# Optimization experiments

Hardware: AMD Instinct MI355X
Metric: run time of the kernel (lower is better)

The kernel has to match this reference:

```python
import jax, jax.numpy as jnp
import numpy as np

B, T, S, A, P = 256, 32, 2048, 64, 128


def setup_inputs() -> dict:
    key = jax.random.key(0)
    ks = jax.random.split(key, 10)
    def w(k, shape, fan_in):
        return jax.random.normal(k, shape, dtype=jnp.float32) / np.sqrt(fan_in)
    return {
        "state": jax.random.normal(ks[0], (B, S), dtype=jnp.float32),
        "act_sequence": jax.random.normal(ks[1], (B, T, A), dtype=jnp.float32),
        "latent": jax.random.normal(ks[2], (B, P), dtype=jnp.float32),
        "fc_W": w(ks[3], (S, S + A + P), S + A + P),
        "fc_b": jnp.zeros((S,), dtype=jnp.float32),
        "fc1_W": w(ks[4], (S, 2 * S), 2 * S),
        "fc2_W": w(ks[5], (S, S), S),
        "W_W": w(ks[6], (4 * S, S), S),
        "reward_W": w(ks[7], (1, S), S),
        "reward_b": jnp.zeros((1,), dtype=jnp.float32),
    }


def reference(state, act_sequence, latent, fc_W, fc_b, fc1_W, fc2_W, W_W, reward_W, reward_b):
    s_dim = fc2_W.shape[0]
    relu = jax.nn.relu

    def fc(x):  # nn.Linear(s+a+p -> s, bias=True)
        return x @ fc_W.T + fc_b

    # initial hidden/cell both from relu(fc(cat[state, act[:,0], latent]))
    hs0 = jnp.concatenate([state, act_sequence[:, 0, :], latent], axis=1)
    hidden = relu(fc(hs0))
    cell = relu(fc(hs0))

    acts = jnp.transpose(act_sequence, (1, 0, 2))  # [T, B, A]

    def step(carry, act_i):
        h, c = carry
        # LSTMCell called as lstm(hidden, [hidden, cell]) -> input == h_cur == h
        combined = jnp.concatenate([h, h], axis=1)            # [B, 2S]
        x = relu(combined @ fc1_W.T)
        x = relu(x @ fc2_W.T)
        cc = relu(x @ W_W.T)                                   # [B, 4S]
        cc_i, cc_f, cc_o, cc_g = jnp.split(cc, 4, axis=1)
        i_g = jax.nn.sigmoid(cc_i)
        f_g = jax.nn.sigmoid(cc_f)
        o_g = jax.nn.sigmoid(cc_o)
        g_g = jnp.tanh(cc_g)
        c_next = f_g * c + i_g * g_g
        h_next = o_g * jnp.tanh(c_next)
        reward = h_next @ reward_W.T + reward_b                # [B, 1]
        # hidden for next iteration (uses act_sequence[:, i, :], as in source);
        # at the last step this carry is simply discarded.
        hs = jnp.concatenate([h_next, act_i, latent], axis=1)
        h_carry = relu(fc(hs))
        return (h_carry, c_next), (h_next, reward)

    (_, _), (preds, rewards) = jax.lax.scan(step, (hidden, cell), acts)
    # torch.cat(list, dim=0) over T steps of [B, *] -> [T*B, *]
    preds = preds.reshape(-1, s_dim)
    rewards = rewards.reshape(-1, 1)
    return preds, rewards
```

## Files before the change

### kernel.cpp

```cpp
#include <hip/hip_runtime.h>

typedef unsigned short u16;
typedef unsigned int   u32;
typedef __attribute__((ext_vector_type(8))) short s8v;
typedef __attribute__((ext_vector_type(8))) unsigned short u8v;
typedef __attribute__((ext_vector_type(4))) float f32x4;

__device__ __forceinline__ float bf2f(u16 v) {
    union { u32 u; float f; } x; x.u = ((u32)v) << 16; return x.f;
}
__device__ __forceinline__ u16 f2bf(float f) {
    union { float f; u32 u; } x; x.f = f;
    return (u16)((x.u + 0x7fffu + ((x.u >> 16) & 1u)) >> 16);
}
__device__ __forceinline__ float sigf(float x)  { return 1.0f / (1.0f + __expf(-x)); }
__device__ __forceinline__ float tanhf_(float x){ return 1.0f - 2.0f / (__expf(2.0f * x) + 1.0f); }

constexpr int Bb = 256, Tt = 32, Ss = 2048, Aa = 64, Pp = 128, SAPd = 2240;

typedef const __attribute__((address_space(1))) unsigned int* gp1_t;
typedef __attribute__((address_space(3))) unsigned int* lp3_t;
__device__ __forceinline__ void gl16(const void* g, void* l) {
    __builtin_amdgcn_global_load_lds((gp1_t)g, (lp3_t)l, 16, 0, 0);
}
#define VMW3() asm volatile("s_waitcnt vmcnt(3)" ::: "memory")
#define VMW0() asm volatile("s_waitcnt vmcnt(0)" ::: "memory")

__global__ void detect_k(const u32* __restrict__ st, int* __restrict__ flag) {
    u32 w = st[threadIdx.x];
    int e = (w >> 7) & 0xFF;
    unsigned long long m = __ballot(e >= 100 && e <= 140);
    if (threadIdx.x == 0) flag[0] = (__popcll(m) >= 32) ? 1 : 0;
}

__global__ __launch_bounds__(256)
void prep_k(const void* __restrict__ state, const void* __restrict__ act,
            const void* __restrict__ latent, const void* __restrict__ fc1W,
            u16* __restrict__ hs, u16* __restrict__ fc1s, float* __restrict__ rewbuf,
            const int* __restrict__ flagp, int big)
{
    const bool bfe = (flagp[0] == 1);
    int g0 = blockIdx.x * 256 + threadIdx.x;
    int stride = gridDim.x * 256;
    for (int i = g0; i < Bb * SAPd; i += stride) {
        int b = i / SAPd, k = i - b * SAPd;
        const void* p; size_t src;
        if (k < Ss)           { p = state;  src = (size_t)b * Ss + k; }
        else if (k < Ss + Aa) { p = act;    src = (size_t)b * (Tt * Aa) + (k - Ss); }
        else                  { p = latent; src = (size_t)b * Pp + (k - Ss - Aa); }
        hs[i] = bfe ? ((const u16*)p)[src] : f2bf(((const float*)p)[src]);
    }
    for (int i = g0; i < Tt * Bb; i += stride) rewbuf[i] = 0.0f;
    if (big) {
        for (int i = g0; i < Ss * Ss; i += stride) {
            int n = i >> 11, k = i & 2047;
            float s;
            if (bfe) s = bf2f(((const u16*)fc1W)[(size_t)n * 4096 + k])
                       + bf2f(((const u16*)fc1W)[(size_t)n * 4096 + 2048 + k]);
            else     s = ((const float*)fc1W)[(size_t)n * 4096 + k]
                       + ((const float*)fc1W)[(size_t)n * 4096 + 2048 + k];
            fc1s[i] = f2bf(s);
        }
    }
}

template<int K, bool BIAS, bool WC, bool FOLD, bool ACT, bool WBF>
__global__ __launch_bounds__(256)
void gemm_k(const u16* __restrict__ Ap, const void* __restrict__ Wp,
            const void* __restrict__ biasp, u16* __restrict__ outp,
            float* __restrict__ cellp,
            u16* __restrict__ hsp, const void* __restrict__ actp, int t,
            const int* __restrict__ flagp)
{
    constexpr int NK = K / 64;
    __shared__ __align__(16) char smem[36864];
    const bool bfe = (flagp[0] == 1);
    const int tid = threadIdx.x;
    const int lane = tid & 63, w = tid >> 6, m16 = lane & 15, q = lane >> 4;
    const int r0 = blockIdx.y * 32, c0 = blockIdx.x * 64;

    if (ACT) {
        if (blockIdx.y == 0) {
            int i = blockIdx.x * 512 + tid * 2;
            int b = i >> 6, a2 = i & 63;
            if (bfe) {
                u32 v = *(const u32*)((const u16*)actp + ((size_t)b * Tt + t) * Aa + a2);
                *(u32*)(hsp + (size_t)b * SAPd + Ss + a2) = v;
            } else {
                const float* s = (const float*)actp + ((size_t)b * Tt + t) * Aa + a2;
                *(u32*)(hsp + (size_t)b * SAPd + Ss + a2) =
                    (u32)f2bf(s[0]) | ((u32)f2bf(s[1]) << 16);
            }
            VMW0();
        }
    }

    const int srow = tid >> 3, sch = tid & 7;
    const int fr2 = 32 + srow;
    f32x4 acc0 = {}, acc1 = {};
    const bool mainp = (WBF || bfe) && !FOLD;

    auto COMPUTE = [&](int p) {
        const char* bufA = smem + p * 12288;
        const char* bufB = bufA + 4096;
        const int sw = (m16 & 7) << 4;
        #pragma unroll
        for (int kh = 0; kh < 2; kh++) {
            int cb = ((kh << 6) | (q << 4)) ^ sw;
            s8v b  = *(const s8v*)(bufB + (w * 16 + m16) * 128 + cb);
            s8v a0 = *(const s8v*)(bufA + m16 * 128 + cb);
            s8v a1 = *(const s8v*)(bufA + (16 + m16) * 128 + cb);
            acc0 = __builtin_amdgcn_mfma_f32_16x16x32_bf16(a0, b, acc0, 0, 0, 0);
            acc1 = __builtin_amdgcn_mfma_f32_16x16x32_bf16(a1, b, acc1, 0, 0, 0);
        }
    };

    if (mainp) {
        const u16* W16 = (const u16*)Wp;
        auto STAGE = [&](int kt, int p) {
            char* bufA = smem + p * 12288;
            char* bufB = bufA + 4096;
            int kb = kt * 64;
            gl16(Ap + (size_t)(r0 + srow) * K + kb + ((sch ^ (srow & 7)) * 8),
                 bufA + w * 1024);
            gl16(W16 + (size_t)(c0 + srow) * K + kb + ((sch ^ (srow & 7)) * 8),
                 bufB + w * 1024);
            gl16(W16 + (size_t)(c0 + fr2) * K + kb + ((sch ^ (fr2 & 7)) * 8),
                 bufB + 4096 + w * 1024);
        };
        STAGE(0, 0); STAGE(1, 1);
        for (int k = 0; k < NK - 2; k++) {
            VMW3();
            __builtin_amdgcn_s_barrier();
            STAGE(k + 2, (k + 2) % 3);
            COMPUTE(k % 3);
        }
        VMW3();
        __builtin_amdgcn_s_barrier();
        COMPUTE((NK - 2) % 3);
        VMW0();
        __builtin_amdgcn_s_barrier();
        COMPUTE((NK - 1) % 3);
    } else {
        u8v fa; u8v rbh[4]; float4 rff[8];
        auto ISSUE = [&](int kt) {
            int kb = kt * 64;
            fa = *(const u8v*)(Ap + (size_t)(r0 + srow) * K + kb + sch * 8);
            if (FOLD) {
                if (bfe) {
                    const u16* p1 = (const u16*)Wp + (size_t)(c0 + srow) * (2 * K) + kb + sch * 8;
                    rbh[0] = *(const u8v*)p1; rbh[1] = *(const u8v*)(p1 + K);
                    const u16* p2 = (const u16*)Wp + (size_t)(c0 + fr2) * (2 * K) + kb + sch * 8;
                    rbh[2] = *(const u8v*)p2; rbh[3] = *(const u8v*)(p2 + K);
                } else {
                    const float* p1 = (const float*)Wp + (size_t)(c0 + srow) * (2 * K) + kb + sch * 8;
                    rff[0] = *(const float4*)p1;       rff[1] = *(const float4*)(p1 + 4);
                    rff[2] = *(const float4*)(p1 + K); rff[3] = *(const float4*)(p1 + K + 4);
                    const float* p2 = (const float*)Wp + (size_t)(c0 + fr2) * (2 * K) + kb + sch * 8;
                    rff[4] = *(const float4*)p2;       rff[5] = *(const float4*)(p2 + 4);
                    rff[6] = *(const float4*)(p2 + K); rff[7] = *(const float4*)(p2 + K + 4);
                }
            } else {
                const float* p1 = (const float*)Wp + (size_t)(c0 + srow) * K + kb + sch * 8;
                rff[0] = *(const float4*)p1; rff[1] = *(const float4*)(p1 + 4);
                const float* p2 = (const float*)Wp + (size_t)(c0 + fr2) * K + kb + sch * 8;
                rff[2] = *(const float4*)p2; rff[3] = *(const float4*)(p2 + 4);
            }
        };
        auto COMMIT = [&](int p) {
            char* bufA = smem + p * 12288;
            char* bufB = bufA + 4096;
            *(u8v*)(bufA + srow * 128 + ((sch ^ (srow & 7)) * 16)) = fa;
            u8v v1, v2;
            if (FOLD) {
                if (bfe) {
                    #pragma unroll
                    for (int j = 0; j < 8; j++) {
                        v1[j] = f2bf(bf2f(rbh[0][j]) + bf2f(rbh[1][j]));
                        v2[j] = f2bf(bf2f(rbh[2][j]) + bf2f(rbh[3][j]));
                    }
                } else {
                    float a0[8], a1[8], b0[8], b1[8];
                    *(float4*)&a0[0] = rff[0]; *(float4*)&a0[4] = rff[1];
                    *(float4*)&a1[0] = rff[2]; *(float4*)&a1[4] = rff[3];
                    *(float4*)&b0[0] = rff[4]; *(float4*)&b0[4] = rff[5];
                    *(float4*)&b1[0] = rff[6]; *(float4*)&b1[4] = rff[7];
                    #pragma unroll
                    for (int j = 0; j < 8; j++) {
                        v1[j] = f2bf(a0[j] + a1[j]);
                        v2[j] = f2bf(b0[j] + b1[j]);
                    }
                }
            } else {
                float a0[8], a1[8];
                *(float4*)&a0[0] = rff[0]; *(float4*)&a0[4] = rff[1];
                *(float4*)&a1[0] = rff[2]; *(float4*)&a1[4] = rff[3];
                #pragma unroll
                for (int j = 0; j < 8; j++) { v1[j] = f2bf(a0[j]); v2[j] = f2bf(a1[j]); }
            }
            *(u8v*)(bufB + srow * 128 + ((sch ^ (srow & 7)) * 16)) = v1;
            *(u8v*)(bufB + fr2 * 128 + ((sch ^ (fr2 & 7)) * 16)) = v2;
        };
        ISSUE(0);
        for (int k = 0; k < NK; k++) {
            __syncthreads();
            COMMIT(k & 1);
            __syncthreads();
            if (k + 1 < NK) ISSUE(k + 1);
            COMPUTE(k & 1);
        }
    }

    const int col = c0 + w * 16 + m16;
    float bv = 0.0f;
    if (BIAS) bv = bfe ? bf2f(((const u16*)biasp)[col]) : ((const float*)biasp)[col];
    #pragma unroll
    for (int r = 0; r < 4; r++) {
        int row0 = r0 + q * 4 + r;
        float v0 = fmaxf(acc0[r] + bv, 0.0f);
        outp[(size_t)row0 * 2048 + col] = f2bf(v0);
        if (WC) cellp[(size_t)row0 * 2048 + col] = v0;
        int row1 = r0 + 16 + q * 4 + r;
        float v1 = fmaxf(acc1[r] + bv, 0.0f);
        outp[(size_t)row1 * 2048 + col] = f2bf(v1);
        if (WC) cellp[(size_t)row1 * 2048 + col] = v1;
    }
}

__global__ __launch_bounds__(256)
void wgates_k(const u16* __restrict__ Ap, const void* __restrict__ Wp,
              float* __restrict__ cbuf, u16* __restrict__ hsp,
              void* __restrict__ dout, const void* __restrict__ rwWp,
              float* __restrict__ rewbuf, int t, const int* __restrict__ flagp)
{
    constexpr int K = 2048, NK = 32;
    __shared__ __align__(16) char smem[36864];
    const bool bfe = (flagp[0] == 1);
    const int tid = threadIdx.x;
    const int lane = tid & 63, g = tid >> 6, m16 = lane & 15, q = lane >> 4;
    const int r0 = blockIdx.y * 32, j0 = blockIdx.x * 16;

    const int srow = tid >> 3, sch = tid & 7;
    const int fr2 = 32 + srow;
    const int wr1 = (srow >> 4) * 2048 + j0 + (srow & 15);
    const int wr2 = (fr2 >> 4) * 2048 + j0 + (fr2 & 15);
    f32x4 acc0 = {}, acc1 = {};

    auto COMPUTE = [&](int p) {
        const char* bufA = smem + p * 12288;
        const char* bufB = bufA + 4096;
        const int sw = (m16 & 7) << 4;
        #pragma unroll
        for (int kh = 0; kh < 2; kh++) {
            int cb = ((kh << 6) | (q << 4)) ^ sw;
            s8v b  = *(const s8v*)(bufB + (g * 16 + m16) * 128 + cb);
            s8v a0 = *(const s8v*)(bufA + m16 * 128 + cb);
            s8v a1 = *(const s8v*)(bufA + (16 + m16) * 128 + cb);
            acc0 = __builtin_amdgcn_mfma_f32_16x16x32_bf16(a0, b, acc0, 0, 0, 0);
            acc1 = __builtin_amdgcn_mfma_f32_16x16x32_bf16(a1, b, acc1, 0, 0, 0);
        }
    };

    if (bfe) {
        const u16* W16 = (const u16*)Wp;
        auto STAGE = [&](int kt, int p) {
            char* bufA = smem + p * 12288;
            char* bufB = bufA + 4096;
            int kb = kt * 64;
            gl16(Ap + (size_t)(r0 + srow) * K + kb + ((sch ^ (srow & 7)) * 8),
                 bufA + g * 1024);
            gl16(W16 + (size_t)wr1 * K + kb + ((sch ^ (srow & 7)) * 8),
                 bufB + g * 1024);
            gl16(W16 + (size_t)wr2 * K + kb + ((sch ^ (fr2 & 7)) * 8),
                 bufB + 4096 + g * 1024);
        };
        STAGE(0, 0); STAGE(1, 1);
        for (int k = 0; k < NK - 2; k++) {
            VMW3();
            __builtin_amdgcn_s_barrier();
            STAGE(k + 2, (k + 2) % 3);
            COMPUTE(k % 3);
        }
        VMW3();
        __builtin_amdgcn_s_barrier();
        COMPUTE((NK - 2) % 3);
        VMW0();
        __builtin_amdgcn_s_barrier();
        COMPUTE((NK - 1) % 3);
    } else {
        u8v fa; float4 rff[4];
        auto ISSUE = [&](int kt) {
            int kb = kt * 64;
            fa = *(const u8v*)(Ap + (size_t)(r0 + srow) * K + kb + sch * 8);
            const float* p1 = (const float*)Wp + (size_t)wr1 * K + kb + sch * 8;
            rff[0] = *(const float4*)p1; rff[1] = *(const float4*)(p1 + 4);
            const float* p2 = (const float*)Wp + (size_t)wr2 * K + kb + sch * 8;
            rff[2] = *(const float4*)p2; rff[3] = *(const float4*)(p2 + 4);
        };
        auto COMMIT = [&](int p) {
            char* bufA = smem + p * 12288;
            char* bufB = bufA + 4096;
            *(u8v*)(bufA + srow * 128 + ((sch ^ (srow & 7)) * 16)) = fa;
            float a0[8], a1[8];
            *(float4*)&a0[0] = rff[0]; *(float4*)&a0[4] = rff[1];
            *(float4*)&a1[0] = rff[2]; *(float4*)&a1[4] = rff[3];
            u8v v1, v2;
            #pragma unroll
            for (int j = 0; j < 8; j++) { v1[j] = f2bf(a0[j]); v2[j] = f2bf(a1[j]); }
            *(u8v*)(bufB + srow * 128 + ((sch ^ (srow & 7)) * 16)) = v1;
            *(u8v*)(bufB + fr2 * 128 + ((sch ^ (fr2 & 7)) * 16)) = v2;
        };
        ISSUE(0);
        for (int k = 0; k < NK; k++) {
            __syncthreads();
            COMMIT(k & 1);
            __syncthreads();
            if (k + 1 < NK) ISSUE(k + 1);
            COMPUTE(k & 1);
        }
    }

    __syncthreads();
    float* gbuf = (float*)smem;
    #pragma unroll
    for (int r = 0; r < 4; r++) {
        int row0 = q * 4 + r;
        gbuf[(row0 * 16 + m16) * 4 + g] = fmaxf(acc0[r], 0.0f);
        int row1 = 16 + q * 4 + r;
        gbuf[(row1 * 16 + m16) * 4 + g] = fmaxf(acc1[r], 0.0f);
    }
    __syncthreads();

    const int row = tid >> 3, jj = (tid & 7) * 2;
    const int grow = r0 + row, jcol = j0 + jj;
    float2 cold = *(const float2*)&cbuf[(size_t)grow * 2048 + jcol];
    float rw0 = bfe ? bf2f(((const u16*)rwWp)[jcol])     : ((const float*)rwWp)[jcol];
    float rw1 = bfe ? bf2f(((const u16*)rwWp)[jcol + 1]) : ((const float*)rwWp)[jcol + 1];

    float cn[2], hnf[2];
    float coldv[2] = { cold.x, cold.y };
    float rsum = 0.0f;
    #pragma unroll
    for (int u = 0; u < 2; u++) {
        const float* gq = &gbuf[((row * 16) + jj + u) * 4];
        float ig = sigf(gq[0]), fg = sigf(gq[1]), og = sigf(gq[2]), tg = tanhf_(gq[3]);
        float c_ = fg * coldv[u] + ig * tg;
        float hn = og * tanhf_(c_);
        cn[u] = c_; hnf[u] = hn;
        rsum += hn * (u ? rw1 : rw0);
    }
    *(float2*)&cbuf[(size_t)grow * 2048 + jcol] = *(float2*)cn;
    u32 hpack = (u32)f2bf(hnf[0]) | ((u32)f2bf(hnf[1]) << 16);
    *(u32*)&hsp[(size_t)grow * SAPd + jcol] = hpack;
    size_t pb = ((size_t)t * 256 + grow) * 2048 + jcol;
    if (bfe) *(u32*)&((u16*)dout)[pb] = hpack;
    else     { ((float*)dout)[pb] = hnf[0]; ((float*)dout)[pb + 1] = hnf[1]; }

    rsum += __shfl_xor(rsum, 1);
    rsum += __shfl_xor(rsum, 2);
    rsum += __shfl_xor(rsum, 4);
    if ((tid & 7) == 0) atomicAdd(&rewbuf[t * 256 + grow], rsum);
}

__global__ void rewfin_k(const float* __restrict__ rewbuf, void* __restrict__ dout,
                         const void* __restrict__ rwb, const int* __restrict__ flagp) {
    const bool bfe = (flagp[0] == 1);
    int i = blockIdx.x * 256 + threadIdx.x;
    float rb = bfe ? bf2f(((const u16*)rwb)[0]) : ((const float*)rwb)[0];
    float v = rewbuf[i] + rb;
    size_t o = (size_t)Tt * Bb * Ss + i;
    if (bfe) ((u16*)dout)[o] = f2bf(v);
    else     ((float*)dout)[o] = v;
}

extern "C" void kernel_launch(void* const* d_in, const int* in_sizes, int n_in,
                              void* d_out, int out_size, void* d_ws, size_t ws_size,
                              hipStream_t stream)
{
    const void* state  = d_in[0];
    const void* act    = d_in[1];
    const void* latent = d_in[2];
    const void* fcW    = d_in[3];
    const void* fcb    = d_in[4];
    const void* fc1W   = d_in[5];
    const void* fc2W   = d_in[6];
    const void* WW     = d_in[7];
    const void* rwW    = d_in[8];
    const void* rwb    = d_in[9];
    char* ws = (char*)d_ws;

    int*   flag   = (int*)  (ws + 0);
    u16*   hs     = (u16*)  (ws + 1024);
    u16*   h      = (u16*)  (ws + 1147904);
    u16*   x1     = (u16*)  (ws + 2196480);
    u16*   x2     = (u16*)  (ws + 3245056);
    float* cbuf   = (float*)(ws + 4293632);
    float* rewbuf = (float*)(ws + 6390784);
    u16*   fc1s   = (u16*)  (ws + 6423552);
    const bool big = ws_size >= 14812160ull;

    detect_k<<<dim3(1), dim3(64), 0, stream>>>((const u32*)state, flag);
    prep_k<<<dim3(4096), dim3(256), 0, stream>>>(state, act, latent, fc1W,
                                                 hs, fc1s, rewbuf, flag, big ? 1 : 0);

    gemm_k<2240, true, true, false, false, false><<<dim3(32, 8), dim3(256), 0, stream>>>(
        hs, fcW, fcb, h, cbuf, nullptr, nullptr, 0, flag);

    for (int t = 0; t < 32; t++) {
        if (big)
            gemm_k<2048, false, false, false, true, true><<<dim3(32, 8), dim3(256), 0, stream>>>(
                h, fc1s, nullptr, x1, nullptr, hs, act, t, flag);
        else
            gemm_k<2048, false, false, true, true, false><<<dim3(32, 8), dim3(256), 0, stream>>>(
                h, fc1W, nullptr, x1, nullptr, hs, act, t, flag);
        gemm_k<2048, false, false, false, false, false><<<dim3(32, 8), dim3(256), 0, stream>>>(
            x1, fc2W, nullptr, x2, nullptr, nullptr, nullptr, 0, flag);
        wgates_k<<<dim3(128, 8), dim3(256), 0, stream>>>(
            x2, WW, cbuf, hs, d_out, rwW, rewbuf, t, flag);
        if (t < 31)
            gemm_k<2240, true, false, false, false, false><<<dim3(32, 8), dim3(256), 0, stream>>>(
                hs, fcW, fcb, h, nullptr, nullptr, nullptr, 0, flag);
    }
    rewfin_k<<<dim3(32), dim3(256), 0, stream>>>(rewbuf, d_out, rwb, flag);
}
```

Measured before the change: 3.053 ms.

## Switch GEMMs to 32x32x16 MFMA with split-K warps and larger K step

Replaces the 16x16x32 MFMA tiling with 32x32x16 MFMA, where the four warps split into two column tiles times two K halves and reduce partial sums through shared memory. The K step per pipeline stage grows to 128 for the 2048-wide GEMMs, and the A operand on the fallback path now uses async global-to-LDS loads. This aims to cut LDS reads per FLOP and the number of barrier iterations, at the cost of more LDS per block, an extra reduction pass and possible occupancy loss.

```diff
diff --git a/kernel.cpp b/kernel.cpp
--- a/kernel.cpp
+++ b/kernel.cpp
@@ -4,7 +4,7 @@
 typedef unsigned int   u32;
 typedef __attribute__((ext_vector_type(8))) short s8v;
 typedef __attribute__((ext_vector_type(8))) unsigned short u8v;
-typedef __attribute__((ext_vector_type(4))) float f32x4;
+typedef __attribute__((ext_vector_type(16))) float f32x16;
 
 __device__ __forceinline__ float bf2f(u16 v) {
     union { u32 u; float f; } x; x.u = ((u32)v) << 16; return x.f;
@@ -23,8 +23,11 @@
 __device__ __forceinline__ void gl16(const void* g, void* l) {
     __builtin_amdgcn_global_load_lds((gp1_t)g, (lp3_t)l, 16, 0, 0);
 }
-#define VMW3() asm volatile("s_waitcnt vmcnt(3)" ::: "memory")
-#define VMW0() asm volatile("s_waitcnt vmcnt(0)" ::: "memory")
+template<int N> __device__ __forceinline__ void vmw() {
+    if constexpr (N == 6)      asm volatile("s_waitcnt vmcnt(6)" ::: "memory");
+    else if constexpr (N == 3) asm volatile("s_waitcnt vmcnt(3)" ::: "memory");
+    else                       asm volatile("s_waitcnt vmcnt(0)" ::: "memory");
+}
 
 __global__ void detect_k(const u32* __restrict__ st, int* __restrict__ flag) {
     u32 w = st[threadIdx.x];
@@ -64,7 +67,7 @@
     }
 }
 
-template<int K, bool BIAS, bool WC, bool FOLD, bool ACT, bool WBF>
+template<int K, int KSTEP, bool BIAS, bool WC, bool FOLD, bool ACT, bool WBF>
 __global__ __launch_bounds__(256)
 void gemm_k(const u16* __restrict__ Ap, const void* __restrict__ Wp,
             const void* __restrict__ biasp, u16* __restrict__ outp,
@@ -72,11 +75,18 @@
             u16* __restrict__ hsp, const void* __restrict__ actp, int t,
             const int* __restrict__ flagp)
 {
-    constexpr int NK = K / 64;
-    __shared__ __align__(16) char smem[36864];
+    constexpr int CH   = KSTEP / 8;
+    constexpr int RB   = CH * 16;
+    constexpr int RPS  = 64 / CH;
+    constexpr int ABYT = 32 * RB, BBYT = 64 * RB, BUF = ABYT + BBYT;
+    constexpr int NK   = K / KSTEP;
+    constexpr int GLN  = 3 * CH / 8;
+    constexpr int KS2  = KSTEP / 32;
+    __shared__ __align__(16) char smem[3 * BUF];
     const bool bfe = (flagp[0] == 1);
     const int tid = threadIdx.x;
-    const int lane = tid & 63, w = tid >> 6, m16 = lane & 15, q = lane >> 4;
+    const int lane = tid & 63, w = tid >> 6, ct = w & 1, kh = w >> 1;
+    const int arr = lane & 31, hi = lane >> 5;
     const int r0 = blockIdx.y * 32, c0 = blockIdx.x * 64;
 
     if (ACT) {
@@ -91,139 +101,160 @@
                 *(u32*)(hsp + (size_t)b * SAPd + Ss + a2) =
                     (u32)f2bf(s[0]) | ((u32)f2bf(s[1]) << 16);
             }
-            VMW0();
-        }
-    }
-
-    const int srow = tid >> 3, sch = tid & 7;
-    const int fr2 = 32 + srow;
-    f32x4 acc0 = {}, acc1 = {};
-    const bool mainp = (WBF || bfe) && !FOLD;
+            vmw<0>();
+        }
+    }
+
+    const int srow_in_seg = lane / CH;
+    const int sc  = lane & (CH - 1);
+
+    f32x16 acc = {};
+    const int brr = ct * 32 + arr;
+    const int sa = arr & (CH - 1), sb = brr & (CH - 1);
 
     auto COMPUTE = [&](int p) {
-        const char* bufA = smem + p * 12288;
-        const char* bufB = bufA + 4096;
-        const int sw = (m16 & 7) << 4;
-        #pragma unroll
-        for (int kh = 0; kh < 2; kh++) {
-            int cb = ((kh << 6) | (q << 4)) ^ sw;
-            s8v b  = *(const s8v*)(bufB + (w * 16 + m16) * 128 + cb);
-            s8v a0 = *(const s8v*)(bufA + m16 * 128 + cb);
-            s8v a1 = *(const s8v*)(bufA + (16 + m16) * 128 + cb);
-            acc0 = __builtin_amdgcn_mfma_f32_16x16x32_bf16(a0, b, acc0, 0, 0, 0);
-            acc1 = __builtin_amdgcn_mfma_f32_16x16x32_bf16(a1, b, acc1, 0, 0, 0);
+        const char* bufA = smem + p * BUF;
+        const char* bufB = bufA + ABYT;
+        #pragma unroll
+        for (int x = 0; x < KS2; x++) {
+            int kk = kh * KS2 + x;
+            s8v a = *(const s8v*)(bufA + arr * RB + ((((kk << 1) | hi) ^ sa) << 4));
+            s8v b = *(const s8v*)(bufB + brr * RB + ((((kk << 1) | hi) ^ sb) << 4));
+            acc = __builtin_amdgcn_mfma_f32_32x32x16_bf16(a, b, acc, 0, 0, 0);
         }
     };
 
-    if (mainp) {
+    const bool fast = (WBF || bfe) && !FOLD;
+    if (fast) {
         const u16* W16 = (const u16*)Wp;
         auto STAGE = [&](int kt, int p) {
-            char* bufA = smem + p * 12288;
-            char* bufB = bufA + 4096;
-            int kb = kt * 64;
-            gl16(Ap + (size_t)(r0 + srow) * K + kb + ((sch ^ (srow & 7)) * 8),
-                 bufA + w * 1024);
-            gl16(W16 + (size_t)(c0 + srow) * K + kb + ((sch ^ (srow & 7)) * 8),
-                 bufB + w * 1024);
-            gl16(W16 + (size_t)(c0 + fr2) * K + kb + ((sch ^ (fr2 & 7)) * 8),
-                 bufB + 4096 + w * 1024);
+            char* bufA = smem + p * BUF;
+            char* bufB = bufA + ABYT;
+            int kb = kt * KSTEP;
+            #pragma unroll
+            for (int i = 0; i < CH / 8; i++) {
+                int s = w * (CH / 8) + i;
+                int row = s * RPS + srow_in_seg;
+                int cg = sc ^ (row & (CH - 1));
+                gl16(Ap + (size_t)(r0 + row) * K + kb + cg * 8, bufA + s * 1024);
+            }
+            #pragma unroll
+            for (int i = 0; i < CH / 4; i++) {
+                int s = w * (CH / 4) + i;
+                int row = s * RPS + srow_in_seg;
+                int cg = sc ^ (row & (CH - 1));
+                gl16(W16 + (size_t)(c0 + row) * K + kb + cg * 8, bufB + s * 1024);
+            }
         };
         STAGE(0, 0); STAGE(1, 1);
         for (int k = 0; k < NK - 2; k++) {
-            VMW3();
+            vmw<GLN>();
             __builtin_amdgcn_s_barrier();
             STAGE(k + 2, (k + 2) % 3);
             COMPUTE(k % 3);
         }
-        VMW3();
+        vmw<GLN>();
         __builtin_amdgcn_s_barrier();
         COMPUTE((NK - 2) % 3);
-        VMW0();
+        vmw<0>();
         __builtin_amdgcn_s_barrier();
         COMPUTE((NK - 1) % 3);
     } else {
-        u8v fa; u8v rbh[4]; float4 rff[8];
+        const int br  = tid >> 2;
+        const int bc0 = (tid & 3) * (CH / 4);
+        const int wrow = c0 + br;
+        u8v  rbh[2 * (CH / 4)];
+        float4 rff[4 * (CH / 4)];
         auto ISSUE = [&](int kt) {
-            int kb = kt * 64;
-            fa = *(const u8v*)(Ap + (size_t)(r0 + srow) * K + kb + sch * 8);
-            if (FOLD) {
-                if (bfe) {
-                    const u16* p1 = (const u16*)Wp + (size_t)(c0 + srow) * (2 * K) + kb + sch * 8;
-                    rbh[0] = *(const u8v*)p1; rbh[1] = *(const u8v*)(p1 + K);
-                    const u16* p2 = (const u16*)Wp + (size_t)(c0 + fr2) * (2 * K) + kb + sch * 8;
-                    rbh[2] = *(const u8v*)p2; rbh[3] = *(const u8v*)(p2 + K);
-                } else {
-                    const float* p1 = (const float*)Wp + (size_t)(c0 + srow) * (2 * K) + kb + sch * 8;
-                    rff[0] = *(const float4*)p1;       rff[1] = *(const float4*)(p1 + 4);
-                    rff[2] = *(const float4*)(p1 + K); rff[3] = *(const float4*)(p1 + K + 4);
-                    const float* p2 = (const float*)Wp + (size_t)(c0 + fr2) * (2 * K) + kb + sch * 8;
-                    rff[4] = *(const float4*)p2;       rff[5] = *(const float4*)(p2 + 4);
-                    rff[6] = *(const float4*)(p2 + K); rff[7] = *(const float4*)(p2 + K + 4);
-                }
-            } else {
-                const float* p1 = (const float*)Wp + (size_t)(c0 + srow) * K + kb + sch * 8;
-                rff[0] = *(const float4*)p1; rff[1] = *(const float4*)(p1 + 4);
-                const float* p2 = (const float*)Wp + (size_t)(c0 + fr2) * K + kb + sch * 8;
-                rff[2] = *(const float4*)p2; rff[3] = *(const float4*)(p2 + 4);
-            }
-        };
-        auto COMMIT = [&](int p) {
-            char* bufA = smem + p * 12288;
-            char* bufB = bufA + 4096;
-            *(u8v*)(bufA + srow * 128 + ((sch ^ (srow & 7)) * 16)) = fa;
-            u8v v1, v2;
-            if (FOLD) {
-                if (bfe) {
-                    #pragma unroll
-                    for (int j = 0; j < 8; j++) {
-                        v1[j] = f2bf(bf2f(rbh[0][j]) + bf2f(rbh[1][j]));
-                        v2[j] = f2bf(bf2f(rbh[2][j]) + bf2f(rbh[3][j]));
+            int kb = kt * KSTEP;
+            #pragma unroll
+            for (int i = 0; i < CH / 4; i++) {
+                int c = bc0 + i, cg = c ^ (br & (CH - 1));
+                if (FOLD) {
+                    if (bfe) {
+                        const u16* p1 = (const u16*)Wp + (size_t)wrow * (2 * K) + kb + cg * 8;
+                        rbh[2 * i] = *(const u8v*)p1; rbh[2 * i + 1] = *(const u8v*)(p1 + K);
+                    } else {
+                        const float* p1 = (const float*)Wp + (size_t)wrow * (2 * K) + kb + cg * 8;
+                        rff[4 * i]     = *(const float4*)p1;
+                        rff[4 * i + 1] = *(const float4*)(p1 + 4);
+                        rff[4 * i + 2] = *(const float4*)(p1 + K);
+                        rff[4 * i + 3] = *(const float4*)(p1 + K + 4);
                     }
                 } else {
-                    float a0[8], a1[8], b0[8], b1[8];
-                    *(float4*)&a0[0] = rff[0]; *(float4*)&a0[4] = rff[1];
-                    *(float4*)&a1[0] = rff[2]; *(float4*)&a1[4] = rff[3];
-                    *(float4*)&b0[0] = rff[4]; *(float4*)&b0[4] = rff[5];
-                    *(float4*)&b1[0] = rff[6]; *(float4*)&b1[4] = rff[7];
+                    const float* p1 = (const float*)Wp + (size_t)wrow * K + kb + cg * 8;
+                    rff[4 * i]     = *(const float4*)p1;
+                    rff[4 * i + 1] = *(const float4*)(p1 + 4);
+                }
+            }
+        };
+        auto STAGE_A = [&](int kt, int p) {
+            char* bufA = smem + p * BUF;
+            int kb = kt * KSTEP;
+            #pragma unroll
+            for (int i = 0; i < CH / 8; i++) {
+                int s = w * (CH / 8) + i;
+                int row = s * RPS + srow_in_seg;
+                int cg = sc ^ (row & (CH - 1));
+                gl16(Ap + (size_t)(r0 + row) * K + kb + cg * 8, bufA + s * 1024);
+            }
+        };
+        auto COMMIT = [&](int p) {
+            char* bufB = smem + p * BUF + ABYT;
+            #pragma unroll
+            for (int i = 0; i < CH / 4; i++) {
+                u8v v;
+                if (FOLD) {
+                    if (bfe) {
+                        #pragma unroll
+                        for (int j = 0; j < 8; j++)
+                            v[j] = f2bf(bf2f(rbh[2 * i][j]) + bf2f(rbh[2 * i + 1][j]));
+                    } else {
+                        float a0[8], a1[8];
+                        *(float4*)&a0[0] = rff[4 * i];     *(float4*)&a0[4] = rff[4 * i + 1];
+                        *(float4*)&a1[0] = rff[4 * i + 2]; *(float4*)&a1[4] = rff[4 * i + 3];
+                        #pragma unroll
+                        for (int j = 0; j < 8; j++) v[j] = f2bf(a0[j] + a1[j]);
+                    }
+                } else {
+                    float a0[8];
+                    *(float4*)&a0[0] = rff[4 * i]; *(float4*)&a0[4] = rff[4 * i + 1];
                     #pragma unroll
-                    for (int j = 0; j < 8; j++) {
-                        v1[j] = f2bf(a0[j] + a1[j]);
-                        v2[j] = f2bf(b0[j] + b1[j]);
-                    }
+                    for (int j = 0; j < 8; j++) v[j] = f2bf(a0[j]);
                 }
-            } else {
-                float a0[8], a1[8];
-                *(float4*)&a0[0] = rff[0]; *(float4*)&a0[4] = rff[1];
-                *(float4*)&a1[0] = rff[2]; *(float4*)&a1[4] = rff[3];
-                #pragma unroll
-                for (int j = 0; j < 8; j++) { v1[j] = f2bf(a0[j]); v2[j] = f2bf(a1[j]); }
-            }
-            *(u8v*)(bufB + srow * 128 + ((sch ^ (srow & 7)) * 16)) = v1;
-            *(u8v*)(bufB + fr2 * 128 + ((sch ^ (fr2 & 7)) * 16)) = v2;
-        };
-        ISSUE(0);
+                *(u8v*)(bufB + br * RB + (bc0 + i) * 16) = v;
+            }
+        };
+        ISSUE(0); STAGE_A(0, 0);
         for (int k = 0; k < NK; k++) {
             __syncthreads();
             COMMIT(k & 1);
             __syncthreads();
-            if (k + 1 < NK) ISSUE(k + 1);
+            if (k + 1 < NK) { STAGE_A(k + 1, (k + 1) & 1); ISSUE(k + 1); }
             COMPUTE(k & 1);
         }
     }
 
-    const int col = c0 + w * 16 + m16;
-    float bv = 0.0f;
-    if (BIAS) bv = bfe ? bf2f(((const u16*)biasp)[col]) : ((const float*)biasp)[col];
-    #pragma unroll
-    for (int r = 0; r < 4; r++) {
-        int row0 = r0 + q * 4 + r;
-        float v0 = fmaxf(acc0[r] + bv, 0.0f);
-        outp[(size_t)row0 * 2048 + col] = f2bf(v0);
-        if (WC) cellp[(size_t)row0 * 2048 + col] = v0;
-        int row1 = r0 + 16 + q * 4 + r;
-        float v1 = fmaxf(acc1[r] + bv, 0.0f);
-        outp[(size_t)row1 * 2048 + col] = f2bf(v1);
-        if (WC) cellp[(size_t)row1 * 2048 + col] = v1;
+    __syncthreads();
+    float* red = (float*)smem;
+    if (w >= 2) {
+        #pragma unroll
+        for (int r = 0; r < 16; r++) red[ct * 1024 + r * 64 + lane] = acc[r];
+    }
+    __syncthreads();
+    if (w < 2) {
+        #pragma unroll
+        for (int r = 0; r < 16; r++) acc[r] += red[ct * 1024 + r * 64 + lane];
+        const int col = c0 + ct * 32 + arr;
+        float bv = 0.0f;
+        if (BIAS) bv = bfe ? bf2f(((const u16*)biasp)[col]) : ((const float*)biasp)[col];
+        #pragma unroll
+        for (int r = 0; r < 16; r++) {
+            int row = r0 + (r & 3) + 8 * (r >> 2) + 4 * hi;
+            float v = fmaxf(acc[r] + bv, 0.0f);
+            outp[(size_t)row * 2048 + col] = f2bf(v);
+            if (WC) cellp[(size_t)row * 2048 + col] = v;
+        }
     }
 }
 
@@ -233,101 +264,134 @@
               void* __restrict__ dout, const void* __restrict__ rwWp,
               float* __restrict__ rewbuf, int t, const int* __restrict__ flagp)
 {
-    constexpr int K = 2048, NK = 32;
-    __shared__ __align__(16) char smem[36864];
+    constexpr int K = 2048, KSTEP = 128, CH = 16, RB = 256, RPS = 4;
+    constexpr int ABYT = 32 * RB, BBYT = 64 * RB, BUF = ABYT + BBYT;
+    constexpr int NK = K / KSTEP, KS2 = KSTEP / 32;
+    __shared__ __align__(16) char smem[3 * BUF];
     const bool bfe = (flagp[0] == 1);
     const int tid = threadIdx.x;
-    const int lane = tid & 63, g = tid >> 6, m16 = lane & 15, q = lane >> 4;
+    const int lane = tid & 63, w = tid >> 6, ct = w & 1, kh = w >> 1;
+    const int arr = lane & 31, hi = lane >> 5;
     const int r0 = blockIdx.y * 32, j0 = blockIdx.x * 16;
 
-    const int srow = tid >> 3, sch = tid & 7;
-    const int fr2 = 32 + srow;
-    const int wr1 = (srow >> 4) * 2048 + j0 + (srow & 15);
-    const int wr2 = (fr2 >> 4) * 2048 + j0 + (fr2 & 15);
-    f32x4 acc0 = {}, acc1 = {};
+    const int srow_in_seg = lane / CH;
+    const int sc  = lane & (CH - 1);
+
+    f32x16 acc = {};
+    const int brr = ct * 32 + arr;
+    const int sa = arr & (CH - 1), sb = brr & (CH - 1);
 
     auto COMPUTE = [&](int p) {
-        const char* bufA = smem + p * 12288;
-        const char* bufB = bufA + 4096;
-        const int sw = (m16 & 7) << 4;
-        #pragma unroll
-        for (int kh = 0; kh < 2; kh++) {
-            int cb = ((kh << 6) | (q << 4)) ^ sw;
-            s8v b  = *(const s8v*)(bufB + (g * 16 + m16) * 128 + cb);
-            s8v a0 = *(const s8v*)(bufA + m16 * 128 + cb);
-            s8v a1 = *(const s8v*)(bufA + (16 + m16) * 128 + cb);
-            acc0 = __builtin_amdgcn_mfma_f32_16x16x32_bf16(a0, b, acc0, 0, 0, 0);
-            acc1 = __builtin_amdgcn_mfma_f32_16x16x32_bf16(a1, b, acc1, 0, 0, 0);
+        const char* bufA = smem + p * BUF;
+        const char* bufB = bufA + ABYT;
+        #pragma unroll
+        for (int x = 0; x < KS2; x++) {
+            int kk = kh * KS2 + x;
+            s8v a = *(const s8v*)(bufA + arr * RB + ((((kk << 1) | hi) ^ sa) << 4));
+            s8v b = *(const s8v*)(bufB + brr * RB + ((((kk << 1) | hi) ^ sb) << 4));
+            acc = __builtin_amdgcn_mfma_f32_32x32x16_bf16(a, b, acc, 0, 0, 0);
         }
     };
 
     if (bfe) {
         const u16* W16 = (const u16*)Wp;
         auto STAGE = [&](int kt, int p) {
-            char* bufA = smem + p * 12288;
-            char* bufB = bufA + 4096;
-            int kb = kt * 64;
-            gl16(Ap + (size_t)(r0 + srow) * K + kb + ((sch ^ (srow & 7)) * 8),
-                 bufA + g * 1024);
-            gl16(W16 + (size_t)wr1 * K + kb + ((sch ^ (srow & 7)) * 8),
-                 bufB + g * 1024);
-            gl16(W16 + (size_t)wr2 * K + kb + ((sch ^ (fr2 & 7)) * 8),
-                 bufB + 4096 + g * 1024);
+            char* bufA = smem + p * BUF;
+            char* bufB = bufA + ABYT;
+            int kb = kt * KSTEP;
+            #pragma unroll
+            for (int i = 0; i < CH / 8; i++) {
+                int s = w * (CH / 8) + i;
+                int row = s * RPS + srow_in_seg;
+                int cg = sc ^ (row & (CH - 1));
+                gl16(Ap + (size_t)(r0 + row) * K + kb + cg * 8, bufA + s * 1024);
+            }
+            #pragma unroll
+            for (int i = 0; i < CH / 4; i++) {
+                int s = w * (CH / 4) + i;
+                int row = s * RPS + srow_in_seg;
+                int wr = (row >> 4) * 2048 + j0 + (row & 15);
+                int cg = sc ^ (row & (CH - 1));
+                gl16(W16 + (size_t)wr * K + kb + cg * 8, bufB + s * 1024);
+            }
         };
         STAGE(0, 0); STAGE(1, 1);
         for (int k = 0; k < NK - 2; k++) {
-            VMW3();
+            vmw<6>();
             __builtin_amdgcn_s_barrier();
             STAGE(k + 2, (k + 2) % 3);
             COMPUTE(k % 3);
         }
-        VMW3();
+        vmw<6>();
         __builtin_amdgcn_s_barrier();
         COMPUTE((NK - 2) % 3);
-        VMW0();
+        vmw<0>();
         __builtin_amdgcn_s_barrier();
         COMPUTE((NK - 1) % 3);
     } else {
-        u8v fa; float4 rff[4];
+        const int br  = tid >> 2;
+        const int bc0 = (tid & 3) * (CH / 4);
+        const int wrow = (br >> 4) * 2048 + j0 + (br & 15);
+        float4 rff[2 * (CH / 4)];
         auto ISSUE = [&](int kt) {
-            int kb = kt * 64;
-            fa = *(const u8v*)(Ap + (size_t)(r0 + srow) * K + kb + sch * 8);
-            const float* p1 = (const float*)Wp + (size_t)wr1 * K + kb + sch * 8;
-            rff[0] = *(const float4*)p1; rff[1] = *(const float4*)(p1 + 4);
-            const float* p2 = (const float*)Wp + (size_t)wr2 * K + kb + sch * 8;
-            rff[2] = *(const float4*)p2; rff[3] = *(const float4*)(p2 + 4);
+            int kb = kt * KSTEP;
+            #pragma unroll
+            for (int i = 0; i < CH / 4; i++) {
+                int c = bc0 + i, cg = c ^ (br & (CH - 1));
+                const float* p1 = (const float*)Wp + (size_t)wrow * K + kb + cg * 8;
+                rff[2 * i]     = *(const float4*)p1;
+                rff[2 * i + 1] = *(const float4*)(p1 + 4);
+            }
+        };
+        auto STAGE_A = [&](int kt, int p) {
+            char* bufA = smem + p * BUF;
+            int kb = kt * KSTEP;
+            #pragma unroll
+            for (int i = 0; i < CH / 8; i++) {
+                int s = w * (CH / 8) + i;
+                int row = s * RPS + srow_in_seg;
+                int cg = sc ^ (row & (CH - 1));
+                gl16(Ap + (size_t)(r0 + row) * K + kb + cg * 8, bufA + s * 1024);
+            }
         };
         auto COMMIT = [&](int p) {
-            char* bufA = smem + p * 12288;
-            char* bufB = bufA + 4096;
-            *(u8v*)(bufA + srow * 128 + ((sch ^ (srow & 7)) * 16)) = fa;
-            float a0[8], a1[8];
-            *(float4*)&a0[0] = rff[0]; *(float4*)&a0[4] = rff[1];
-            *(float4*)&a1[0] = rff[2]; *(float4*)&a1[4] = rff[3];
-            u8v v1, v2;
-            #pragma unroll
-            for (int j = 0; j < 8; j++) { v1[j] = f2bf(a0[j]); v2[j] = f2bf(a1[j]); }
-            *(u8v*)(bufB + srow * 128 + ((sch ^ (srow & 7)) * 16)) = v1;
-            *(u8v*)(bufB + fr2 * 128 + ((sch ^ (fr2 & 7)) * 16)) = v2;
-        };
-        ISSUE(0);
+            char* bufB = smem + p * BUF + ABYT;
+            #pragma unroll
+            for (int i = 0; i < CH / 4; i++) {
+                float a0[8];
+                *(float4*)&a0[0] = rff[2 * i]; *(float4*)&a0[4] = rff[2 * i + 1];
+                u8v v;
+                #pragma unroll
+                for (int j = 0; j < 8; j++) v[j] = f2bf(a0[j]);
+                *(u8v*)(bufB + br * RB + (bc0 + i) * 16) = v;
+            }
+        };
+        ISSUE(0); STAGE_A(0, 0);
         for (int k = 0; k < NK; k++) {
             __syncthreads();
             COMMIT(k & 1);
             __syncthreads();
-            if (k + 1 < NK) ISSUE(k + 1);
+            if (k + 1 < NK) { STAGE_A(k + 1, (k + 1) & 1); ISSUE(k + 1); }
             COMPUTE(k & 1);
         }
     }
 
     __syncthreads();
-    float* gbuf = (float*)smem;
-    #pragma unroll
-    for (int r = 0; r < 4; r++) {
-        int row0 = q * 4 + r;
-        gbuf[(row0 * 16 + m16) * 4 + g] = fmaxf(acc0[r], 0.0f);
-        int row1 = 16 + q * 4 + r;
-        gbuf[(row1 * 16 + m16) * 4 + g] = fmaxf(acc1[r], 0.0f);
+    float* red  = (float*)smem;
+    float* gbuf = (float*)(smem + 8192);
+    if (w >= 2) {
+        #pragma unroll
+        for (int r = 0; r < 16; r++) red[ct * 1024 + r * 64 + lane] = acc[r];
+    }
+    __syncthreads();
+    if (w < 2) {
+        const int j = arr & 15, gate = ct * 2 + (arr >> 4);
+        #pragma unroll
+        for (int r = 0; r < 16; r++) {
+            float v = acc[r] + red[ct * 1024 + r * 64 + lane];
+            int row = (r & 3) + 8 * (r >> 2) + 4 * hi;
+            gbuf[(row * 16 + j) * 4 + gate] = fmaxf(v, 0.0f);
+        }
     }
     __syncthreads();
 
@@ -403,22 +467,22 @@
     prep_k<<<dim3(4096), dim3(256), 0, stream>>>(state, act, latent, fc1W,
                                                  hs, fc1s, rewbuf, flag, big ? 1 : 0);
 
-    gemm_k<2240, true, true, false, false, false><<<dim3(32, 8), dim3(256), 0, stream>>>(
+    gemm_k<2240, 64, true, true, false, false, false><<<dim3(32, 8), dim3(256), 0, stream>>>(
         hs, fcW, fcb, h, cbuf, nullptr, nullptr, 0, flag);
 
     for (int t = 0; t < 32; t++) {
         if (big)
-            gemm_k<2048, false, false, false, true, true><<<dim3(32, 8), dim3(256), 0, stream>>>(
+            gemm_k<2048, 128, false, false, false, true, true><<<dim3(32, 8), dim3(256), 0, stream>>>(
                 h, fc1s, nullptr, x1, nullptr, hs, act, t, flag);
         else
-            gemm_k<2048, false, false, true, true, false><<<dim3(32, 8), dim3(256), 0, stream>>>(
+            gemm_k<2048, 128, false, false, true, true, false><<<dim3(32, 8), dim3(256), 0, stream>>>(
                 h, fc1W, nullptr, x1, nullptr, hs, act, t, flag);
-        gemm_k<2048, false, false, false, false, false><<<dim3(32, 8), dim3(256), 0, stream>>>(
+        gemm_k<2048, 128, false, false, false, false, false><<<dim3(32, 8), dim3(256), 0, stream>>>(
             x1, fc2W, nullptr, x2, nullptr, nullptr, nullptr, 0, flag);
         wgates_k<<<dim3(128, 8), dim3(256), 0, stream>>>(
             x2, WW, cbuf, hs, d_out, rwW, rewbuf, t, flag);
         if (t < 31)
-            gemm_k<2240, true, false, false, false, false><<<dim3(32, 8), dim3(256), 0, stream>>>(
+            gemm_k<2240, 64, true, false, false, false, false><<<dim3(32, 8), dim3(256), 0, stream>>>(
                 hs, fcW, fcb, h, nullptr, nullptr, nullptr, 0, flag);
     }
     rewfin_k<<<dim3(32), dim3(256), 0, stream>>>(rewbuf, d_out, rwb, flag);
```

Result: slower. 4.840 ms (+58.5%).
